# Kernel optimization log

Measured on AMD Instinct MI355X. Metric: run time of the kernel, lower is better.

The kernel has to match this reference:

```python
import jax, jax.numpy as jnp
import numpy as np

HEAD_DIM = 64
SCALE = HEAD_DIM ** -0.5
NUM_HEADS = 16


def setup_inputs() -> dict:
    key = jax.random.key(0)
    k1, k2, k3, k4 = jax.random.split(key, 4)
    dim = 1024
    query = jax.random.normal(k1, (8, 512, dim), dtype=jnp.float32)
    memory = jax.random.normal(k2, (8, 512, dim), dtype=jnp.float32)
    # nn.Linear weights are [out, in]; scale like default init
    W_Q = jax.random.normal(k3, (dim, dim), dtype=jnp.float32) * (dim ** -0.5)
    W_K = jax.random.normal(k4, (dim, dim), dtype=jnp.float32) * (dim ** -0.5)
    return {"query": query, "memory": memory, "W_Q": W_Q, "W_K": W_K}


def reference(query, memory, W_Q, W_K):
    # Q: [K, Lq, E], K: [B, Lk, E]  (E = H * D)
    Q = query @ W_Q.T
    Km = memory @ W_K.T
    Kb, Lq, E = Q.shape
    Bb, Lk, _ = Km.shape
    Qh = Q.reshape(Kb, Lq, NUM_HEADS, HEAD_DIM).transpose(0, 2, 1, 3)  # K H q D
    Kh = Km.reshape(Bb, Lk, NUM_HEADS, HEAD_DIM).transpose(0, 2, 1, 3)  # B H k D
    # logits: [B, K, H, q, k]
    logits = jnp.einsum('ahqd,bhkd->bahqk', Qh, Kh) * SCALE
    energies = jax.nn.logsumexp(logits, axis=-2) / SCALE  # [B, K, H, k]
    energies = energies.mean(axis=1)  # [B, H, k]
    return energies
```

## Files before the change

### kernel.cpp

```cpp
#include <hip/hip_runtime.h>
#include <hip/hip_bf16.h>

typedef short short8 __attribute__((ext_vector_type(8)));
typedef float f32x4 __attribute__((ext_vector_type(4)));
typedef unsigned short u16;

__device__ __forceinline__ unsigned short f2bf(float f) {
  unsigned int u = __float_as_uint(f);
  u += 0x7fffu + ((u >> 16) & 1u);
  return (unsigned short)(u >> 16);
}

__device__ __forceinline__ void glds16(const void* g, void* l) {
  __builtin_amdgcn_global_load_lds(
      (const __attribute__((address_space(1))) unsigned int*)g,
      (__attribute__((address_space(3))) unsigned int*)l, 16, 0, 0);
}

__device__ __forceinline__ void drain_then_sync() {
  __builtin_amdgcn_s_waitcnt(0);
  __syncthreads();
}

__global__ __launch_bounds__(256) void prep(const float4* __restrict__ q,
                                            const float4* __restrict__ m,
                                            const float4* __restrict__ wq,
                                            const float4* __restrict__ wk,
                                            ushort4* __restrict__ qb,
                                            ushort4* __restrict__ mb,
                                            ushort4* __restrict__ wqb,
                                            ushort4* __restrict__ wkb,
                                            float4* __restrict__ out0) {
  const int i = blockIdx.x * 256 + threadIdx.x;
  const float c = 0.18033688011112042f;
  if (i < 1048576) {
    float4 v = q[i];
    ushort4 o; o.x = f2bf(v.x); o.y = f2bf(v.y); o.z = f2bf(v.z); o.w = f2bf(v.w);
    qb[i] = o;
  } else if (i < 2097152) {
    float4 v = m[i - 1048576];
    ushort4 o; o.x = f2bf(v.x); o.y = f2bf(v.y); o.z = f2bf(v.z); o.w = f2bf(v.w);
    mb[i - 1048576] = o;
  } else if (i < 2359296) {
    float4 v = wq[i - 2097152];
    ushort4 o; o.x = f2bf(v.x * c); o.y = f2bf(v.y * c); o.z = f2bf(v.z * c); o.w = f2bf(v.w * c);
    wqb[i - 2097152] = o;
  } else if (i < 2621440) {
    float4 v = wk[i - 2359296];
    ushort4 o; o.x = f2bf(v.x); o.y = f2bf(v.y); o.z = f2bf(v.z); o.w = f2bf(v.w);
    wkb[i - 2359296] = o;
  } else if (i < 2637824) {
    out0[i - 2621440] = (float4){0.f, 0.f, 0.f, 0.f};
  }
}

__global__ __launch_bounds__(512) void gemm_db(const u16* __restrict__ A0,
                                               const u16* __restrict__ B0,
                                               u16* __restrict__ C0,
                                               const u16* __restrict__ A1,
                                               const u16* __restrict__ B1,
                                               u16* __restrict__ C1) {
  __shared__ u16 As[3][128 * 32];
  __shared__ u16 Bs[3][128 * 32];
  const int zz = blockIdx.x & 1;
  const u16* A = zz ? A1 : A0;
  const u16* B = zz ? B1 : B0;
  u16* C = zz ? C1 : C0;
  const int t = threadIdx.x;
  const int lane = t & 63, wave = t >> 6;
  const int l15 = lane & 15, quad = lane >> 4;
  const int mb = (blockIdx.x >> 1) * 128;
  const int nb = blockIdx.y * 128;
  const int wm = (wave & 1) * 64;
  const int wn = (wave >> 1) * 32;

  const int srow = lane >> 2;
  const int sq = (lane & 3) ^ (srow & 3) ^ ((srow >> 2) & 3);
  const size_t arow = (size_t)(mb + wave * 16 + srow) * 1024 + sq * 8;
  const size_t brow = (size_t)(nb + wave * 16 + srow) * 1024 + sq * 8;
  const int ldst = wave * 512 + lane * 8;

  const int sw2 = (l15 & 3) ^ ((l15 >> 2) & 3);
  const int rcol = (quad ^ sw2) * 8;

  f32x4 acc[4][2];
#pragma unroll
  for (int i = 0; i < 4; i++)
#pragma unroll
    for (int j = 0; j < 2; j++) acc[i][j] = (f32x4){0.f, 0.f, 0.f, 0.f};

  glds16(A + arow, &As[0][ldst]);
  glds16(B + brow, &Bs[0][ldst]);
  glds16(A + arow + 32, &As[1][ldst]);
  glds16(B + brow + 32, &Bs[1][ldst]);

#pragma unroll
  for (int it = 0; it < 32; ++it) {
    if (it != 31) asm volatile("s_waitcnt vmcnt(2)" ::: "memory");
    else          asm volatile("s_waitcnt vmcnt(0)" ::: "memory");
    __builtin_amdgcn_s_barrier();
    __builtin_amdgcn_sched_barrier(0);
    if (it <= 29) {
      const int bf_ = (it + 2) % 3;
      glds16(A + arow + (size_t)(it + 2) * 32, &As[bf_][ldst]);
      glds16(B + brow + (size_t)(it + 2) * 32, &Bs[bf_][ldst]);
    }
    const u16* as = As[it % 3];
    const u16* bs = Bs[it % 3];
    short8 af[4], bfr[2];
#pragma unroll
    for (int mi = 0; mi < 4; mi++)
      af[mi] = *(const short8*)&as[(wm + mi * 16 + l15) * 32 + rcol];
#pragma unroll
    for (int ni = 0; ni < 2; ni++)
      bfr[ni] = *(const short8*)&bs[(wn + ni * 16 + l15) * 32 + rcol];
#pragma unroll
    for (int mi = 0; mi < 4; mi++)
#pragma unroll
      for (int ni = 0; ni < 2; ni++)
        acc[mi][ni] = __builtin_amdgcn_mfma_f32_16x16x32_bf16(
            af[mi], bfr[ni], acc[mi][ni], 0, 0, 0);
  }

#pragma unroll
  for (int mi = 0; mi < 4; mi++)
#pragma unroll
    for (int r = 0; r < 4; r++) {
      const int row = mb + wm + mi * 16 + quad * 4 + r;
      const size_t base = (size_t)row * 1024 + nb + wn;
#pragma unroll
      for (int ni = 0; ni < 2; ni++)
        C[base + ni * 16 + l15] = f2bf(acc[mi][ni][r]);
    }
}

__global__ __launch_bounds__(256) void attn_lse2(const u16* __restrict__ Qp,
                                                 const u16* __restrict__ Kp,
                                                 float* __restrict__ out) {
  __shared__ u16 qs[2][64 * 64];
  const int t = threadIdx.x;
  const int lane = t & 63, wave = t >> 6;
  const int l15 = lane & 15, quad = lane >> 4;
  const int kt = blockIdx.x & 1, aa = blockIdx.x >> 1;
  const int h = blockIdx.y, b = blockIdx.z;
  const int kwave = kt * 256 + wave * 64;

  short8 klo[4], khi[4];
#pragma unroll
  for (int tt = 0; tt < 4; tt++) {
    const short8* kg = (const short8*)(Kp + (size_t)(b * 512 + kwave + tt * 16 + l15) * 1024
                                       + h * 64 + quad * 8);
    klo[tt] = kg[0];
    khi[tt] = kg[4];
  }

  const int srow = lane >> 3;
  const int scol = ((lane & 7) ^ srow) * 8;
  const u16* qbase = Qp + (size_t)(aa * 512) * 1024 + h * 64;

  const int sw = l15 & 7;
  const int colLo = (quad ^ sw) * 8;
  const int colHi = ((4 + quad) ^ sw) * 8;
  const int rrow = l15 * 64;

  float cs0 = 0.f, cs1 = 0.f, cs2 = 0.f, cs3 = 0.f;

#pragma unroll
  for (int j = 0; j < 2; j++) {
    const int mi_ = wave * 2 + j;
    glds16(qbase + (size_t)(mi_ * 8 + srow) * 1024 + scol, &qs[0][mi_ * 512 + lane * 8]);
  }

  for (int i = 0; i < 8; i++) {
    drain_then_sync();
    if (i < 7) {
#pragma unroll
      for (int j = 0; j < 2; j++) {
        const int mi_ = wave * 2 + j;
        glds16(qbase + (size_t)((i + 1) * 64 + mi_ * 8 + srow) * 1024 + scol,
               &qs[(i + 1) & 1][mi_ * 512 + lane * 8]);
      }
    }
    const u16* buf = qs[i & 1];
#pragma unroll
    for (int qt = 0; qt < 4; qt++) {
      short8 alo = *(const short8*)&buf[qt * 1024 + rrow + colLo];
      short8 ahi = *(const short8*)&buf[qt * 1024 + rrow + colHi];
      f32x4 ac0 = (f32x4){0.f, 0.f, 0.f, 0.f};
      f32x4 ac1 = ac0, ac2 = ac0, ac3 = ac0;
      ac0 = __builtin_amdgcn_mfma_f32_16x16x32_bf16(alo, klo[0], ac0, 0, 0, 0);
      ac0 = __builtin_amdgcn_mfma_f32_16x16x32_bf16(ahi, khi[0], ac0, 0, 0, 0);
      ac1 = __builtin_amdgcn_mfma_f32_16x16x32_bf16(alo, klo[1], ac1, 0, 0, 0);
      ac1 = __builtin_amdgcn_mfma_f32_16x16x32_bf16(ahi, khi[1], ac1, 0, 0, 0);
      ac2 = __builtin_amdgcn_mfma_f32_16x16x32_bf16(alo, klo[2], ac2, 0, 0, 0);
      ac2 = __builtin_amdgcn_mfma_f32_16x16x32_bf16(ahi, khi[2], ac2, 0, 0, 0);
      ac3 = __builtin_amdgcn_mfma_f32_16x16x32_bf16(alo, klo[3], ac3, 0, 0, 0);
      ac3 = __builtin_amdgcn_mfma_f32_16x16x32_bf16(ahi, khi[3], ac3, 0, 0, 0);
#pragma unroll
      for (int r = 0; r < 4; r++) {
        cs0 += __builtin_amdgcn_exp2f(ac0[r]);
        cs1 += __builtin_amdgcn_exp2f(ac1[r]);
        cs2 += __builtin_amdgcn_exp2f(ac2[r]);
        cs3 += __builtin_amdgcn_exp2f(ac3[r]);
      }
    }
  }
  cs0 += __shfl_xor(cs0, 16); cs0 += __shfl_xor(cs0, 32);
  cs1 += __shfl_xor(cs1, 16); cs1 += __shfl_xor(cs1, 32);
  cs2 += __shfl_xor(cs2, 16); cs2 += __shfl_xor(cs2, 32);
  cs3 += __shfl_xor(cs3, 16); cs3 += __shfl_xor(cs3, 32);
  const float v = quad == 0 ? cs0 : quad == 1 ? cs1 : quad == 2 ? cs2 : cs3;
  atomicAdd(out + (size_t)b * 8192 + h * 512 + kwave + quad * 16 + l15, __logf(v));
}

extern "C" void kernel_launch(void* const* d_in, const int* in_sizes, int n_in,
                              void* d_out, int out_size, void* d_ws, size_t ws_size,
                              hipStream_t stream) {
  const float* query  = (const float*)d_in[0];
  const float* memory = (const float*)d_in[1];
  const float* wq     = (const float*)d_in[2];
  const float* wk     = (const float*)d_in[3];
  float* out = (float*)d_out;

  char* ws = (char*)d_ws;
  const size_t MB = 1024 * 1024;
  u16* qb  = (u16*)(ws);
  u16* mb_ = (u16*)(ws + 8  * MB);
  u16* wqb = (u16*)(ws + 16 * MB);
  u16* wkb = (u16*)(ws + 18 * MB);
  u16* Qp  = (u16*)(ws + 20 * MB);
  u16* Kp  = (u16*)(ws + 28 * MB);

  prep<<<10304, 256, 0, stream>>>((const float4*)query, (const float4*)memory,
                                  (const float4*)wq, (const float4*)wk,
                                  (ushort4*)qb, (ushort4*)mb_, (ushort4*)wqb,
                                  (ushort4*)wkb, (float4*)d_out);
  gemm_db<<<dim3(64, 8), 512, 0, stream>>>(qb, wqb, Qp, mb_, wkb, Kp);
  attn_lse2<<<dim3(16, 16, 8), 256, 0, stream>>>(Qp, Kp, out);
}
```

Measured before the change: 151.8 us.

## Fuse prep, projection GEMM and LSE attention into one persistent kernel with grid barriers

Merges the three launches into a single 512-block kernel that runs the bf16 conversion, the Q/K projection GEMM and the logsumexp attention stage, separated by software grid barriers built on atomic counters. The aim is to remove launch gaps and tail effects between kernels. Each attention block now covers all 512 keys for two query batches, with 8 waves instead of 4. The barrier depends on all 512 blocks being co-resident and has a spin timeout that could silently break correctness. A memset for the barrier counters is added on the stream.

```diff
diff --git a/kernel.cpp b/kernel.cpp
--- a/kernel.cpp
+++ b/kernel.cpp
@@ -22,195 +22,204 @@
   __syncthreads();
 }
 
-__global__ __launch_bounds__(256) void prep(const float4* __restrict__ q,
-                                            const float4* __restrict__ m,
-                                            const float4* __restrict__ wq,
-                                            const float4* __restrict__ wk,
-                                            ushort4* __restrict__ qb,
-                                            ushort4* __restrict__ mb,
-                                            ushort4* __restrict__ wqb,
-                                            ushort4* __restrict__ wkb,
-                                            float4* __restrict__ out0) {
-  const int i = blockIdx.x * 256 + threadIdx.x;
-  const float c = 0.18033688011112042f;
-  if (i < 1048576) {
-    float4 v = q[i];
-    ushort4 o; o.x = f2bf(v.x); o.y = f2bf(v.y); o.z = f2bf(v.z); o.w = f2bf(v.w);
-    qb[i] = o;
-  } else if (i < 2097152) {
-    float4 v = m[i - 1048576];
-    ushort4 o; o.x = f2bf(v.x); o.y = f2bf(v.y); o.z = f2bf(v.z); o.w = f2bf(v.w);
-    mb[i - 1048576] = o;
-  } else if (i < 2359296) {
-    float4 v = wq[i - 2097152];
-    ushort4 o; o.x = f2bf(v.x * c); o.y = f2bf(v.y * c); o.z = f2bf(v.z * c); o.w = f2bf(v.w * c);
-    wqb[i - 2097152] = o;
-  } else if (i < 2621440) {
-    float4 v = wk[i - 2359296];
-    ushort4 o; o.x = f2bf(v.x); o.y = f2bf(v.y); o.z = f2bf(v.z); o.w = f2bf(v.w);
-    wkb[i - 2359296] = o;
-  } else if (i < 2637824) {
-    out0[i - 2621440] = (float4){0.f, 0.f, 0.f, 0.f};
-  }
-}
-
-__global__ __launch_bounds__(512) void gemm_db(const u16* __restrict__ A0,
-                                               const u16* __restrict__ B0,
-                                               u16* __restrict__ C0,
-                                               const u16* __restrict__ A1,
-                                               const u16* __restrict__ B1,
-                                               u16* __restrict__ C1) {
-  __shared__ u16 As[3][128 * 32];
-  __shared__ u16 Bs[3][128 * 32];
-  const int zz = blockIdx.x & 1;
-  const u16* A = zz ? A1 : A0;
-  const u16* B = zz ? B1 : B0;
-  u16* C = zz ? C1 : C0;
+__device__ __forceinline__ void gridbar(unsigned* c, unsigned n) {
+  __syncthreads();
+  if (threadIdx.x == 0) {
+    __threadfence();
+    __hip_atomic_fetch_add(c, 1u, __ATOMIC_RELEASE, __HIP_MEMORY_SCOPE_AGENT);
+    unsigned spins = 0;
+    while (__hip_atomic_load(c, __ATOMIC_ACQUIRE, __HIP_MEMORY_SCOPE_AGENT) < n) {
+      __builtin_amdgcn_s_sleep(2);
+      if (++spins > 2000000u) break;
+    }
+  }
+  __syncthreads();
+  __threadfence();
+}
+
+__global__ __launch_bounds__(512, 4) void fused_all(
+    const float4* __restrict__ q, const float4* __restrict__ m,
+    const float4* __restrict__ wq, const float4* __restrict__ wk,
+    u16* __restrict__ qb, u16* __restrict__ mb_,
+    u16* __restrict__ wqb, u16* __restrict__ wkb,
+    u16* __restrict__ Qp, u16* __restrict__ Kp,
+    float* __restrict__ out, unsigned* __restrict__ bars) {
+  __shared__ u16 smem[24576];
+  const int bid = blockIdx.x;
   const int t = threadIdx.x;
   const int lane = t & 63, wave = t >> 6;
   const int l15 = lane & 15, quad = lane >> 4;
-  const int mb = (blockIdx.x >> 1) * 128;
-  const int nb = blockIdx.y * 128;
-  const int wm = (wave & 1) * 64;
-  const int wn = (wave >> 1) * 32;
-
-  const int srow = lane >> 2;
-  const int sq = (lane & 3) ^ (srow & 3) ^ ((srow >> 2) & 3);
-  const size_t arow = (size_t)(mb + wave * 16 + srow) * 1024 + sq * 8;
-  const size_t brow = (size_t)(nb + wave * 16 + srow) * 1024 + sq * 8;
-  const int ldst = wave * 512 + lane * 8;
-
-  const int sw2 = (l15 & 3) ^ ((l15 >> 2) & 3);
-  const int rcol = (quad ^ sw2) * 8;
-
-  f32x4 acc[4][2];
-#pragma unroll
-  for (int i = 0; i < 4; i++)
-#pragma unroll
-    for (int j = 0; j < 2; j++) acc[i][j] = (f32x4){0.f, 0.f, 0.f, 0.f};
-
-  glds16(A + arow, &As[0][ldst]);
-  glds16(B + brow, &Bs[0][ldst]);
-  glds16(A + arow + 32, &As[1][ldst]);
-  glds16(B + brow + 32, &Bs[1][ldst]);
-
-#pragma unroll
-  for (int it = 0; it < 32; ++it) {
-    if (it != 31) asm volatile("s_waitcnt vmcnt(2)" ::: "memory");
-    else          asm volatile("s_waitcnt vmcnt(0)" ::: "memory");
-    __builtin_amdgcn_s_barrier();
-    __builtin_amdgcn_sched_barrier(0);
-    if (it <= 29) {
-      const int bf_ = (it + 2) % 3;
-      glds16(A + arow + (size_t)(it + 2) * 32, &As[bf_][ldst]);
-      glds16(B + brow + (size_t)(it + 2) * 32, &Bs[bf_][ldst]);
-    }
-    const u16* as = As[it % 3];
-    const u16* bs = Bs[it % 3];
-    short8 af[4], bfr[2];
+
+  {
+    const float c = 0.18033688011112042f;
+    for (int i = bid * 512 + t; i < 2637824; i += 262144) {
+      if (i < 1048576) {
+        float4 v = q[i];
+        ushort4 o; o.x = f2bf(v.x); o.y = f2bf(v.y); o.z = f2bf(v.z); o.w = f2bf(v.w);
+        ((ushort4*)qb)[i] = o;
+      } else if (i < 2097152) {
+        float4 v = m[i - 1048576];
+        ushort4 o; o.x = f2bf(v.x); o.y = f2bf(v.y); o.z = f2bf(v.z); o.w = f2bf(v.w);
+        ((ushort4*)mb_)[i - 1048576] = o;
+      } else if (i < 2359296) {
+        float4 v = wq[i - 2097152];
+        ushort4 o; o.x = f2bf(v.x * c); o.y = f2bf(v.y * c);
+        o.z = f2bf(v.z * c); o.w = f2bf(v.w * c);
+        ((ushort4*)wqb)[i - 2097152] = o;
+      } else if (i < 2621440) {
+        float4 v = wk[i - 2359296];
+        ushort4 o; o.x = f2bf(v.x); o.y = f2bf(v.y); o.z = f2bf(v.z); o.w = f2bf(v.w);
+        ((ushort4*)wkb)[i - 2359296] = o;
+      } else {
+        ((float4*)out)[i - 2621440] = (float4){0.f, 0.f, 0.f, 0.f};
+      }
+    }
+  }
+  gridbar(bars + 0, 512);
+
+  {
+    u16* const As0 = smem;
+    u16* const Bs0 = smem + 12288;
+    const int x = bid & 63, y = bid >> 6;
+    const int zz = x & 1;
+    const u16* A = zz ? mb_ : qb;
+    const u16* B = zz ? wkb : wqb;
+    u16* C = zz ? Kp : Qp;
+    const int mb = (x >> 1) * 128;
+    const int nb = y * 128;
+    const int wm = (wave & 1) * 64;
+    const int wn = (wave >> 1) * 32;
+
+    const int srow = lane >> 2;
+    const int sq = (lane & 3) ^ (srow & 3) ^ ((srow >> 2) & 3);
+    const size_t arow = (size_t)(mb + wave * 16 + srow) * 1024 + sq * 8;
+    const size_t brow = (size_t)(nb + wave * 16 + srow) * 1024 + sq * 8;
+    const int ldst = wave * 512 + lane * 8;
+
+    const int sw2 = (l15 & 3) ^ ((l15 >> 2) & 3);
+    const int rcol = (quad ^ sw2) * 8;
+
+    f32x4 acc[4][2];
+#pragma unroll
+    for (int i = 0; i < 4; i++)
+#pragma unroll
+      for (int j = 0; j < 2; j++) acc[i][j] = (f32x4){0.f, 0.f, 0.f, 0.f};
+
+    glds16(A + arow, &As0[ldst]);
+    glds16(B + brow, &Bs0[ldst]);
+    glds16(A + arow + 32, &As0[4096 + ldst]);
+    glds16(B + brow + 32, &Bs0[4096 + ldst]);
+
+#pragma unroll
+    for (int it = 0; it < 32; ++it) {
+      if (it != 31) asm volatile("s_waitcnt vmcnt(2)" ::: "memory");
+      else          asm volatile("s_waitcnt vmcnt(0)" ::: "memory");
+      __builtin_amdgcn_s_barrier();
+      __builtin_amdgcn_sched_barrier(0);
+      if (it <= 29) {
+        const int bf_ = (it + 2) % 3;
+        glds16(A + arow + (size_t)(it + 2) * 32, &As0[bf_ * 4096 + ldst]);
+        glds16(B + brow + (size_t)(it + 2) * 32, &Bs0[bf_ * 4096 + ldst]);
+      }
+      const u16* as = &As0[(it % 3) * 4096];
+      const u16* bs = &Bs0[(it % 3) * 4096];
+      short8 af[4], bfr[2];
+#pragma unroll
+      for (int mi = 0; mi < 4; mi++)
+        af[mi] = *(const short8*)&as[(wm + mi * 16 + l15) * 32 + rcol];
+#pragma unroll
+      for (int ni = 0; ni < 2; ni++)
+        bfr[ni] = *(const short8*)&bs[(wn + ni * 16 + l15) * 32 + rcol];
+#pragma unroll
+      for (int mi = 0; mi < 4; mi++)
+#pragma unroll
+        for (int ni = 0; ni < 2; ni++)
+          acc[mi][ni] = __builtin_amdgcn_mfma_f32_16x16x32_bf16(
+              af[mi], bfr[ni], acc[mi][ni], 0, 0, 0);
+    }
+
 #pragma unroll
     for (int mi = 0; mi < 4; mi++)
-      af[mi] = *(const short8*)&as[(wm + mi * 16 + l15) * 32 + rcol];
-#pragma unroll
-    for (int ni = 0; ni < 2; ni++)
-      bfr[ni] = *(const short8*)&bs[(wn + ni * 16 + l15) * 32 + rcol];
-#pragma unroll
-    for (int mi = 0; mi < 4; mi++)
-#pragma unroll
-      for (int ni = 0; ni < 2; ni++)
-        acc[mi][ni] = __builtin_amdgcn_mfma_f32_16x16x32_bf16(
-            af[mi], bfr[ni], acc[mi][ni], 0, 0, 0);
-  }
-
-#pragma unroll
-  for (int mi = 0; mi < 4; mi++)
-#pragma unroll
-    for (int r = 0; r < 4; r++) {
-      const int row = mb + wm + mi * 16 + quad * 4 + r;
-      const size_t base = (size_t)row * 1024 + nb + wn;
-#pragma unroll
-      for (int ni = 0; ni < 2; ni++)
-        C[base + ni * 16 + l15] = f2bf(acc[mi][ni][r]);
-    }
-}
-
-__global__ __launch_bounds__(256) void attn_lse2(const u16* __restrict__ Qp,
-                                                 const u16* __restrict__ Kp,
-                                                 float* __restrict__ out) {
-  __shared__ u16 qs[2][64 * 64];
-  const int t = threadIdx.x;
-  const int lane = t & 63, wave = t >> 6;
-  const int l15 = lane & 15, quad = lane >> 4;
-  const int kt = blockIdx.x & 1, aa = blockIdx.x >> 1;
-  const int h = blockIdx.y, b = blockIdx.z;
-  const int kwave = kt * 256 + wave * 64;
-
-  short8 klo[4], khi[4];
-#pragma unroll
-  for (int tt = 0; tt < 4; tt++) {
-    const short8* kg = (const short8*)(Kp + (size_t)(b * 512 + kwave + tt * 16 + l15) * 1024
-                                       + h * 64 + quad * 8);
-    klo[tt] = kg[0];
-    khi[tt] = kg[4];
-  }
-
-  const int srow = lane >> 3;
-  const int scol = ((lane & 7) ^ srow) * 8;
-  const u16* qbase = Qp + (size_t)(aa * 512) * 1024 + h * 64;
-
-  const int sw = l15 & 7;
-  const int colLo = (quad ^ sw) * 8;
-  const int colHi = ((4 + quad) ^ sw) * 8;
-  const int rrow = l15 * 64;
-
-  float cs0 = 0.f, cs1 = 0.f, cs2 = 0.f, cs3 = 0.f;
-
-#pragma unroll
-  for (int j = 0; j < 2; j++) {
-    const int mi_ = wave * 2 + j;
-    glds16(qbase + (size_t)(mi_ * 8 + srow) * 1024 + scol, &qs[0][mi_ * 512 + lane * 8]);
-  }
-
-  for (int i = 0; i < 8; i++) {
-    drain_then_sync();
-    if (i < 7) {
-#pragma unroll
-      for (int j = 0; j < 2; j++) {
-        const int mi_ = wave * 2 + j;
-        glds16(qbase + (size_t)((i + 1) * 64 + mi_ * 8 + srow) * 1024 + scol,
-               &qs[(i + 1) & 1][mi_ * 512 + lane * 8]);
-      }
-    }
-    const u16* buf = qs[i & 1];
-#pragma unroll
-    for (int qt = 0; qt < 4; qt++) {
-      short8 alo = *(const short8*)&buf[qt * 1024 + rrow + colLo];
-      short8 ahi = *(const short8*)&buf[qt * 1024 + rrow + colHi];
-      f32x4 ac0 = (f32x4){0.f, 0.f, 0.f, 0.f};
-      f32x4 ac1 = ac0, ac2 = ac0, ac3 = ac0;
-      ac0 = __builtin_amdgcn_mfma_f32_16x16x32_bf16(alo, klo[0], ac0, 0, 0, 0);
-      ac0 = __builtin_amdgcn_mfma_f32_16x16x32_bf16(ahi, khi[0], ac0, 0, 0, 0);
-      ac1 = __builtin_amdgcn_mfma_f32_16x16x32_bf16(alo, klo[1], ac1, 0, 0, 0);
-      ac1 = __builtin_amdgcn_mfma_f32_16x16x32_bf16(ahi, khi[1], ac1, 0, 0, 0);
-      ac2 = __builtin_amdgcn_mfma_f32_16x16x32_bf16(alo, klo[2], ac2, 0, 0, 0);
-      ac2 = __builtin_amdgcn_mfma_f32_16x16x32_bf16(ahi, khi[2], ac2, 0, 0, 0);
-      ac3 = __builtin_amdgcn_mfma_f32_16x16x32_bf16(alo, klo[3], ac3, 0, 0, 0);
-      ac3 = __builtin_amdgcn_mfma_f32_16x16x32_bf16(ahi, khi[3], ac3, 0, 0, 0);
 #pragma unroll
       for (int r = 0; r < 4; r++) {
-        cs0 += __builtin_amdgcn_exp2f(ac0[r]);
-        cs1 += __builtin_amdgcn_exp2f(ac1[r]);
-        cs2 += __builtin_amdgcn_exp2f(ac2[r]);
-        cs3 += __builtin_amdgcn_exp2f(ac3[r]);
-      }
-    }
-  }
-  cs0 += __shfl_xor(cs0, 16); cs0 += __shfl_xor(cs0, 32);
-  cs1 += __shfl_xor(cs1, 16); cs1 += __shfl_xor(cs1, 32);
-  cs2 += __shfl_xor(cs2, 16); cs2 += __shfl_xor(cs2, 32);
-  cs3 += __shfl_xor(cs3, 16); cs3 += __shfl_xor(cs3, 32);
-  const float v = quad == 0 ? cs0 : quad == 1 ? cs1 : quad == 2 ? cs2 : cs3;
-  atomicAdd(out + (size_t)b * 8192 + h * 512 + kwave + quad * 16 + l15, __logf(v));
+        const int row = mb + wm + mi * 16 + quad * 4 + r;
+        const size_t base = (size_t)row * 1024 + nb + wn;
+#pragma unroll
+        for (int ni = 0; ni < 2; ni++)
+          C[base + ni * 16 + l15] = f2bf(acc[mi][ni][r]);
+      }
+  }
+  gridbar(bars + 1, 512);
+
+  {
+    u16* const qs0 = smem;
+    const int b = bid & 7;
+    const int h = (bid >> 3) & 15;
+    const int sub = bid >> 7;
+    const int kwave = wave * 64;
+
+    short8 klo[4], khi[4];
+#pragma unroll
+    for (int tt = 0; tt < 4; tt++) {
+      const short8* kg = (const short8*)(Kp + (size_t)(b * 512 + kwave + tt * 16 + l15) * 1024
+                                         + h * 64 + quad * 8);
+      klo[tt] = kg[0];
+      khi[tt] = kg[4];
+    }
+
+    const int srow = lane >> 3;
+    const int scol = ((lane & 7) ^ srow) * 8;
+    const int sw = l15 & 7;
+    const int colLo = (quad ^ sw) * 8;
+    const int colHi = ((4 + quad) ^ sw) * 8;
+    const int rrow = l15 * 64;
+
+    for (int a2 = 0; a2 < 2; ++a2) {
+      const int aa = sub * 2 + a2;
+      const u16* qbase = Qp + (size_t)(aa * 512) * 1024 + h * 64;
+      float cs0 = 0.f, cs1 = 0.f, cs2 = 0.f, cs3 = 0.f;
+
+      glds16(qbase + (size_t)(wave * 8 + srow) * 1024 + scol,
+             &qs0[wave * 512 + lane * 8]);
+
+      for (int i = 0; i < 8; i++) {
+        drain_then_sync();
+        if (i < 7) {
+          glds16(qbase + (size_t)((i + 1) * 64 + wave * 8 + srow) * 1024 + scol,
+                 &qs0[((i + 1) & 1) * 4096 + wave * 512 + lane * 8]);
+        }
+        const u16* buf = &qs0[(i & 1) * 4096];
+#pragma unroll
+        for (int qt = 0; qt < 4; qt++) {
+          short8 alo = *(const short8*)&buf[qt * 1024 + rrow + colLo];
+          short8 ahi = *(const short8*)&buf[qt * 1024 + rrow + colHi];
+          f32x4 ac0 = (f32x4){0.f, 0.f, 0.f, 0.f};
+          f32x4 ac1 = ac0, ac2 = ac0, ac3 = ac0;
+          ac0 = __builtin_amdgcn_mfma_f32_16x16x32_bf16(alo, klo[0], ac0, 0, 0, 0);
+          ac0 = __builtin_amdgcn_mfma_f32_16x16x32_bf16(ahi, khi[0], ac0, 0, 0, 0);
+          ac1 = __builtin_amdgcn_mfma_f32_16x16x32_bf16(alo, klo[1], ac1, 0, 0, 0);
+          ac1 = __builtin_amdgcn_mfma_f32_16x16x32_bf16(ahi, khi[1], ac1, 0, 0, 0);
+          ac2 = __builtin_amdgcn_mfma_f32_16x16x32_bf16(alo, klo[2], ac2, 0, 0, 0);
+          ac2 = __builtin_amdgcn_mfma_f32_16x16x32_bf16(ahi, khi[2], ac2, 0, 0, 0);
+          ac3 = __builtin_amdgcn_mfma_f32_16x16x32_bf16(alo, klo[3], ac3, 0, 0, 0);
+          ac3 = __builtin_amdgcn_mfma_f32_16x16x32_bf16(ahi, khi[3], ac3, 0, 0, 0);
+#pragma unroll
+          for (int r = 0; r < 4; r++) {
+            cs0 += __builtin_amdgcn_exp2f(ac0[r]);
+            cs1 += __builtin_amdgcn_exp2f(ac1[r]);
+            cs2 += __builtin_amdgcn_exp2f(ac2[r]);
+            cs3 += __builtin_amdgcn_exp2f(ac3[r]);
+          }
+        }
+      }
+      cs0 += __shfl_xor(cs0, 16); cs0 += __shfl_xor(cs0, 32);
+      cs1 += __shfl_xor(cs1, 16); cs1 += __shfl_xor(cs1, 32);
+      cs2 += __shfl_xor(cs2, 16); cs2 += __shfl_xor(cs2, 32);
+      cs3 += __shfl_xor(cs3, 16); cs3 += __shfl_xor(cs3, 32);
+      const float v = quad == 0 ? cs0 : quad == 1 ? cs1 : quad == 2 ? cs2 : cs3;
+      atomicAdd(out + (size_t)b * 8192 + h * 512 + kwave + quad * 16 + l15, __logf(v));
+    }
+  }
 }
 
 extern "C" void kernel_launch(void* const* d_in, const int* in_sizes, int n_in,
@@ -230,11 +239,11 @@
   u16* wkb = (u16*)(ws + 18 * MB);
   u16* Qp  = (u16*)(ws + 20 * MB);
   u16* Kp  = (u16*)(ws + 28 * MB);
-
-  prep<<<10304, 256, 0, stream>>>((const float4*)query, (const float4*)memory,
-                                  (const float4*)wq, (const float4*)wk,
-                                  (ushort4*)qb, (ushort4*)mb_, (ushort4*)wqb,
-                                  (ushort4*)wkb, (float4*)d_out);
-  gemm_db<<<dim3(64, 8), 512, 0, stream>>>(qb, wqb, Qp, mb_, wkb, Kp);
-  attn_lse2<<<dim3(16, 16, 8), 256, 0, stream>>>(Qp, Kp, out);
-}
+  unsigned* bars = (unsigned*)(ws + 36 * MB);
+
+  hipMemsetAsync(bars, 0, 16, stream);
+  fused_all<<<512, 512, 0, stream>>>(
+      (const float4*)query, (const float4*)memory,
+      (const float4*)wq, (const float4*)wk,
+      qb, mb_, wqb, wkb, Qp, Kp, out, bars);
+}
```

After: 427.7 us. 2.82x slower.
